# Performance work log

Measured on AMD Instinct MI355X. Metric: run time of the kernel, lower is better.

## Reference

```python
import jax, jax.numpy as jnp
import numpy as np

N, D = 8192, 1024

def setup_inputs() -> dict:
    key = jax.random.key(0)
    ks = jax.random.split(key, 7)
    s = 1.0 / np.sqrt(D)
    return {
        "sent_mat": jax.random.normal(ks[0], (N, D), dtype=jnp.float32),
        "indicator": 0,
        "Wq": jax.random.normal(ks[1], (D, D), dtype=jnp.float32) * s,
        "bq": jax.random.normal(ks[2], (D,), dtype=jnp.float32) * s,
        "Wk": jax.random.normal(ks[3], (D, D), dtype=jnp.float32) * s,
        "bk": jax.random.normal(ks[4], (D,), dtype=jnp.float32) * s,
        "Wv": jax.random.normal(ks[5], (D, D), dtype=jnp.float32) * s,
        "bv": jax.random.normal(ks[6], (D,), dtype=jnp.float32) * s,
    }

def reference(sent_mat, indicator, Wq, bq, Wk, bk, Wv, bv):
    # torch.nn.Linear: y = x @ W.T + b
    Q = sent_mat @ Wq.T + bq            # [N, D]
    K = sent_mat @ Wk.T + bk            # [N, D]
    V = sent_mat @ Wv.T + bv            # [N, D]
    sim = Q @ K.T                       # [N, N]
    if indicator == 0:                  # custom score inversion
        sim = 1.0 - sim
    sim_norm = sim / jnp.sqrt(jnp.asarray(D, dtype=sim.dtype))
    # NOTE: softmax over dim=0 (columns normalized over rows), unconventional
    attn_w = jax.nn.softmax(sim_norm, axis=0)   # [N, N]
    attn_out = attn_w @ V               # [N, D]
    return (attn_out, attn_w)
```

## Files before the change

### kernel.cpp

```cpp
#include <hip/hip_runtime.h>

#define NT 8192
#define DM 1024

typedef unsigned short u16;
typedef __bf16 bf16x8 __attribute__((ext_vector_type(8)));
typedef float f32x4 __attribute__((ext_vector_type(4)));
typedef u16 u16x8 __attribute__((ext_vector_type(8)));

__device__ __forceinline__ u16 f2bf(float f) {
  union { float f; unsigned u; } v; v.f = f;
  unsigned r = v.u + 0x7fffu + ((v.u >> 16) & 1u);
  return (u16)(r >> 16);
}
__device__ __forceinline__ float bf2f(u16 h) {
  union { unsigned u; float f; } v; v.u = ((unsigned)h) << 16;
  return v.f;
}

__device__ __forceinline__ void stage16(const u16* g, u16* lds_wave_uniform) {
  __builtin_amdgcn_global_load_lds(
      (const __attribute__((address_space(1))) unsigned int*)g,
      (__attribute__((address_space(3))) unsigned int*)lds_wave_uniform, 16, 0, 0);
}

__global__ void cvt_all_kernel(const float* __restrict__ X, const float* __restrict__ Wq,
                               const float* __restrict__ Wk, const float* __restrict__ Wv,
                               u16* __restrict__ Xb, u16* __restrict__ Wqb,
                               u16* __restrict__ Wkb, u16* __restrict__ Wvb) {
  const int NX = NT * DM / 4;
  const int NW = DM * DM / 4;
  const int total = NX + 3 * NW;
  int i = blockIdx.x * blockDim.x + threadIdx.x;
  int stride = gridDim.x * blockDim.x;
  for (; i < total; i += stride) {
    const float* src; u16* dst; int j;
    if (i < NX)               { src = X;  dst = Xb;  j = i; }
    else if (i < NX + NW)     { src = Wq; dst = Wqb; j = i - NX; }
    else if (i < NX + 2 * NW) { src = Wk; dst = Wkb; j = i - NX - NW; }
    else                      { src = Wv; dst = Wvb; j = i - NX - 2 * NW; }
    float4 v = reinterpret_cast<const float4*>(src)[j];
    ushort4 o;
    o.x = f2bf(v.x); o.y = f2bf(v.y); o.z = f2bf(v.z); o.w = f2bf(v.w);
    reinterpret_cast<ushort4*>(dst)[j] = o;
  }
}

__global__ __launch_bounds__(512, 2)
void qkt_exp_256(const u16* __restrict__ Q, const u16* __restrict__ Kmat, int K,
                 u16* __restrict__ E, float* __restrict__ cs,
                 const int* __restrict__ indp) {
  __shared__ u16 AT[2][256 * 64];
  __shared__ u16 BT[2][256 * 64];
  const int t = threadIdx.x;
  const int l = t & 63;
  const int w = t >> 6;
  const int wm = w >> 2;
  const int wn = w & 3;
  const int r16 = l & 15;
  const int half = l >> 4;

  const int gx = gridDim.x;
  const int nwg = gx * gridDim.y;
  int lin = blockIdx.y * gx + blockIdx.x;
  if ((nwg & 7) == 0) lin = (lin & 7) * (nwg >> 3) + (lin >> 3);
  const int bx = lin % gx;
  const int by = lin / gx;
  const size_t brow = (size_t)by * 256;
  const size_t bcol = (size_t)bx * 256;

  const int srow = w * 8 + (l >> 3);
  const int kel = ((l & 7) ^ (l >> 3)) * 8;
  const int ntiles = K >> 6;

  f32x4 acc[8][4] = {};

#pragma unroll
  for (int q = 0; q < 4; ++q) {
    stage16(Q    + (brow + q * 64 + srow) * (size_t)K + kel, &AT[0][q * 4096 + w * 512]);
    stage16(Kmat + (bcol + q * 64 + srow) * (size_t)K + kel, &BT[0][q * 4096 + w * 512]);
  }
  __syncthreads();

  for (int tt = 0; tt < ntiles; ++tt) {
    const int cur = tt & 1;
    const int nxt = cur ^ 1;
    const int k1 = (tt + 1) << 6;
    const bool more = (tt + 1 < ntiles);
#pragma unroll
    for (int p = 0; p < 4; ++p) {
      if (p == 0 && more) {
#pragma unroll
        for (int q = 0; q < 4; ++q)
          stage16(Q + (brow + q * 64 + srow) * (size_t)K + (k1 + kel),
                  &AT[nxt][q * 4096 + w * 512]);
      }
      if (p == 1 && more) {
#pragma unroll
        for (int q = 0; q < 4; ++q)
          stage16(Kmat + (bcol + q * 64 + srow) * (size_t)K + (k1 + kel),
                  &BT[nxt][q * 4096 + w * 512]);
      }
      bf16x8 af[4][2], bfr[2][2];
#pragma unroll
      for (int m = 0; m < 4; ++m) {
        const int row = wm * 128 + (p >> 1) * 64 + m * 16 + r16;
#pragma unroll
        for (int kk = 0; kk < 2; ++kk) {
          const int slot = (half + 4 * kk) ^ (r16 & 7);
          af[m][kk] = *reinterpret_cast<const bf16x8*>(&AT[cur][row * 64 + slot * 8]);
        }
      }
#pragma unroll
      for (int n = 0; n < 2; ++n) {
        const int row = wn * 64 + (p & 1) * 32 + n * 16 + r16;
#pragma unroll
        for (int kk = 0; kk < 2; ++kk) {
          const int slot = (half + 4 * kk) ^ (r16 & 7);
          bfr[n][kk] = *reinterpret_cast<const bf16x8*>(&BT[cur][row * 64 + slot * 8]);
        }
      }
      __builtin_amdgcn_s_setprio(1);
#pragma unroll
      for (int m = 0; m < 4; ++m)
#pragma unroll
        for (int n = 0; n < 2; ++n)
#pragma unroll
          for (int kk = 0; kk < 2; ++kk)
            acc[(p >> 1) * 4 + m][(p & 1) * 2 + n] = __builtin_amdgcn_mfma_f32_16x16x32_bf16(
                af[m][kk], bfr[n][kk], acc[(p >> 1) * 4 + m][(p & 1) * 2 + n], 0, 0, 0);
      __builtin_amdgcn_s_setprio(0);
      __builtin_amdgcn_sched_barrier(0);
    }
    __syncthreads();
  }

  const bool flip = (*indp == 0);
  const float cexp = 0.045084220027780106f;
  float csum[4] = {0.f, 0.f, 0.f, 0.f};
#pragma unroll
  for (int mg = 0; mg < 8; ++mg) {
#pragma unroll
    for (int ng = 0; ng < 4; ++ng) {
#pragma unroll
      for (int q = 0; q < 4; ++q) {
        float s = acc[mg][ng][q];
        float x = flip ? (1.0f - s) : s;
        float e = exp2f(x * cexp);
        size_t row = brow + wm * 128 + mg * 16 + half * 4 + q;
        size_t col = bcol + wn * 64 + ng * 16 + r16;
        E[row * NT + col] = f2bf(e);
        csum[ng] += e;
      }
    }
  }
#pragma unroll
  for (int ng = 0; ng < 4; ++ng) {
    float s = csum[ng];
    s += __shfl_xor(s, 16);
    s += __shfl_xor(s, 32);
    if (l < 16) atomicAdd(&cs[bcol + wn * 64 + ng * 16 + l], s);
  }
}

template<int EPI>
__global__ __launch_bounds__(512, 2)
void mega_bt(const u16* __restrict__ A, const u16* __restrict__ B, int K, int ldo,
             const float* __restrict__ bias, u16* __restrict__ obf,
             float* __restrict__ of32, float* __restrict__ cs,
             float* __restrict__ wf32, const int* __restrict__ indp) {
  __shared__ u16 AT[3][256 * 64];
  __shared__ u16 BT[3][128 * 64];
  const int t = threadIdx.x;
  const int l = t & 63;
  const int w = t >> 6;
  const int wm = w >> 2;
  const int wn = w & 3;
  const int r16 = l & 15;
  const int half = l >> 4;

  const int gx = gridDim.x;
  const int nwg = gx * gridDim.y;
  int lin = blockIdx.y * gx + blockIdx.x;
  if ((nwg & 7) == 0) lin = (lin & 7) * (nwg >> 3) + (lin >> 3);
  const int bx = lin % gx;
  const int by = lin / gx;
  const size_t brow = (size_t)by * 256;
  const size_t bcol = (size_t)bx * 128;

  const int srow = w * 8 + (l >> 3);
  const int kel = ((l & 7) ^ (l >> 3)) * 8;
  const int nt = K >> 6;

  f32x4 acc[8][2] = {};

#define STAGE(tile, buf)                                                              \
  {                                                                                   \
    const int k0_ = (tile) << 6;                                                      \
    _Pragma("unroll")                                                                 \
    for (int q = 0; q < 4; ++q)                                                       \
      stage16(A + (brow + q * 64 + srow) * (size_t)K + (k0_ + kel),                   \
              &AT[buf][q * 4096 + w * 512]);                                          \
    _Pragma("unroll")                                                                 \
    for (int q = 0; q < 2; ++q)                                                       \
      stage16(B + (bcol + q * 64 + srow) * (size_t)K + (k0_ + kel),                   \
              &BT[buf][q * 4096 + w * 512]);                                          \
  }

  STAGE(0, 0);
  STAGE(1, 1);

  for (int tt = 0; tt < nt; ++tt) {
    const int cur = tt % 3;
    if (tt < nt - 1) asm volatile("s_waitcnt vmcnt(6)" ::: "memory");
    else             asm volatile("s_waitcnt vmcnt(0)" ::: "memory");
    __builtin_amdgcn_s_barrier();
    __builtin_amdgcn_sched_barrier(0);
    if (tt + 2 < nt) STAGE(tt + 2, (tt + 2) % 3);
    __builtin_amdgcn_sched_barrier(0);

    bf16x8 bfr[2][2];
#pragma unroll
    for (int n = 0; n < 2; ++n) {
      const int row = wn * 32 + n * 16 + r16;
#pragma unroll
      for (int kk = 0; kk < 2; ++kk) {
        const int slot = (half + 4 * kk) ^ (r16 & 7);
        bfr[n][kk] = *reinterpret_cast<const bf16x8*>(&BT[cur][row * 64 + slot * 8]);
      }
    }
#pragma unroll
    for (int p = 0; p < 2; ++p) {
      bf16x8 af[4][2];
#pragma unroll
      for (int m = 0; m < 4; ++m) {
        const int row = wm * 128 + p * 64 + m * 16 + r16;
#pragma unroll
        for (int kk = 0; kk < 2; ++kk) {
          const int slot = (half + 4 * kk) ^ (r16 & 7);
          af[m][kk] = *reinterpret_cast<const bf16x8*>(&AT[cur][row * 64 + slot * 8]);
        }
      }
      __builtin_amdgcn_s_setprio(1);
#pragma unroll
      for (int m = 0; m < 4; ++m)
#pragma unroll
        for (int n = 0; n < 2; ++n)
#pragma unroll
          for (int kk = 0; kk < 2; ++kk)
            acc[p * 4 + m][n] = __builtin_amdgcn_mfma_f32_16x16x32_bf16(
                af[m][kk], bfr[n][kk], acc[p * 4 + m][n], 0, 0, 0);
      __builtin_amdgcn_s_setprio(0);
      __builtin_amdgcn_sched_barrier(0);
    }

    if constexpr (EPI == 3) {
      if ((tt >> 4) == bx) {
        const int kg = (tt << 6) + l;
        const float invc = 1.0f / cs[kg];
#pragma unroll
        for (int wi = 0; wi < 32; ++wi) {
          const int row = w * 32 + wi;
          const int slot = (l >> 3) ^ (row & 7);
          u16 ev = AT[cur][row * 64 + slot * 8 + (l & 7)];
          wf32[(brow + row) * (size_t)NT + kg] = bf2f(ev) * invc;
        }
      }
    }
  }
#undef STAGE

  if constexpr (EPI == 0) {
#pragma unroll
    for (int mg = 0; mg < 8; ++mg) {
#pragma unroll
      for (int n = 0; n < 2; ++n) {
        const int cc = wn * 32 + n * 16 + r16;
        const float bv = bias[bcol + cc];
#pragma unroll
        for (int q = 0; q < 4; ++q) {
          size_t row = brow + wm * 128 + mg * 16 + half * 4 + q;
          obf[row * (size_t)ldo + bcol + cc] = f2bf(acc[mg][n][q] + bv);
        }
      }
    }
  } else {
#pragma unroll
    for (int mg = 0; mg < 8; ++mg) {
#pragma unroll
      for (int n = 0; n < 2; ++n) {
#pragma unroll
        for (int q = 0; q < 4; ++q) {
          size_t row = brow + wm * 128 + mg * 16 + half * 4 + q;
          size_t col = bcol + wn * 32 + n * 16 + r16;
          of32[row * (size_t)ldo + col] = acc[mg][n][q];
        }
      }
    }
  }
}

template<int EPI, int AF32, int BF32>
__global__ __launch_bounds__(256)
void gemm_bt(const void* __restrict__ Av, const void* __restrict__ Bv, int K, int ldo,
             const float* __restrict__ bias, u16* __restrict__ obf,
             float* __restrict__ of32, const int* __restrict__ indp) {
  __shared__ u16 As[128 * 32];
  __shared__ u16 Bs[128 * 32];
  const int t = threadIdx.x;
  const int l = t & 63;
  const int w = t >> 6;
  const int wr = w >> 1;
  const int wc = w & 1;
  const int r16 = l & 15;
  const int half = l >> 4;

  const int gx = gridDim.x;
  const int nwg = gx * gridDim.y;
  int lin = blockIdx.y * gx + blockIdx.x;
  if ((nwg & 7) == 0) lin = (lin & 7) * (nwg >> 3) + (lin >> 3);
  const int bx = lin % gx;
  const int by = lin / gx;

  const size_t brow = (size_t)by * 128;
  const size_t bcol = (size_t)bx * 128;
  const int kel = (l & 3) * 8;
  const int lrow = l >> 2;

  f32x4 acc[4][4] = {};

  for (int k0 = 0; k0 < K; k0 += 32) {
#pragma unroll
    for (int c = 0; c < 2; ++c) {
      const int seg = c * 4 + w;
      const int r = seg * 16 + lrow;
      if constexpr (AF32) {
        const float* ga = (const float*)Av + (brow + r) * (size_t)K + (k0 + kel);
        float4 u0 = *reinterpret_cast<const float4*>(ga);
        float4 u1 = *reinterpret_cast<const float4*>(ga + 4);
        u16x8 o;
        o[0] = f2bf(u0.x); o[1] = f2bf(u0.y); o[2] = f2bf(u0.z); o[3] = f2bf(u0.w);
        o[4] = f2bf(u1.x); o[5] = f2bf(u1.y); o[6] = f2bf(u1.z); o[7] = f2bf(u1.w);
        *reinterpret_cast<u16x8*>(&As[seg * 512 + l * 8]) = o;
      } else {
        const u16* ga = (const u16*)Av + (brow + r) * (size_t)K + (k0 + kel);
        stage16(ga, &As[seg * 512]);
      }
      if constexpr (BF32) {
        const float* gb = (const float*)Bv + (bcol + r) * (size_t)K + (k0 + kel);
        float4 u0 = *reinterpret_cast<const float4*>(gb);
        float4 u1 = *reinterpret_cast<const float4*>(gb + 4);
        u16x8 o;
        o[0] = f2bf(u0.x); o[1] = f2bf(u0.y); o[2] = f2bf(u0.z); o[3] = f2bf(u0.w);
        o[4] = f2bf(u1.x); o[5] = f2bf(u1.y); o[6] = f2bf(u1.z); o[7] = f2bf(u1.w);
        *reinterpret_cast<u16x8*>(&Bs[seg * 512 + l * 8]) = o;
      } else {
        const u16* gb = (const u16*)Bv + (bcol + r) * (size_t)K + (k0 + kel);
        stage16(gb, &Bs[seg * 512]);
      }
    }
    __syncthreads();
    bf16x8 af[4], bfv[4];
#pragma unroll
    for (int m = 0; m < 4; ++m)
      af[m] = *reinterpret_cast<const bf16x8*>(&As[(wr * 64 + m * 16 + r16) * 32 + half * 8]);
#pragma unroll
    for (int n = 0; n < 4; ++n)
      bfv[n] = *reinterpret_cast<const bf16x8*>(&Bs[(wc * 64 + n * 16 + r16) * 32 + half * 8]);
#pragma unroll
    for (int m = 0; m < 4; ++m)
#pragma unroll
      for (int n = 0; n < 4; ++n)
        acc[m][n] = __builtin_amdgcn_mfma_f32_16x16x32_bf16(af[m], bfv[n], acc[m][n], 0, 0, 0);
    __syncthreads();
  }

  const int crow0 = wr * 64 + half * 4;
  const int ccol0 = wc * 64 + r16;

  if constexpr (EPI == 0) {
#pragma unroll
    for (int m = 0; m < 4; ++m) {
#pragma unroll
      for (int n = 0; n < 4; ++n) {
        const int cc = ccol0 + n * 16;
        const float bv = bias[bcol + cc];
#pragma unroll
        for (int q = 0; q < 4; ++q) {
          size_t idx = (brow + crow0 + m * 16 + q) * (size_t)ldo + (bcol + cc);
          obf[idx] = f2bf(acc[m][n][q] + bv);
        }
      }
    }
  } else if constexpr (EPI == 1) {
    const bool flip = (*indp == 0);
    const float cexp = 0.045084220027780106f;
#pragma unroll
    for (int m = 0; m < 4; ++m) {
#pragma unroll
      for (int n = 0; n < 4; ++n) {
        const int cc = ccol0 + n * 16;
#pragma unroll
        for (int q = 0; q < 4; ++q) {
          float s = acc[m][n][q];
          float x = flip ? (1.0f - s) : s;
          size_t idx = (brow + crow0 + m * 16 + q) * (size_t)ldo + (bcol + cc);
          of32[idx] = exp2f(x * cexp);
        }
      }
    }
  } else {
#pragma unroll
    for (int m = 0; m < 4; ++m) {
#pragma unroll
      for (int n = 0; n < 4; ++n) {
        const int cc = ccol0 + n * 16;
#pragma unroll
        for (int q = 0; q < 4; ++q) {
          size_t idx = (brow + crow0 + m * 16 + q) * (size_t)ldo + (bcol + cc);
          of32[idx] = acc[m][n][q];
        }
      }
    }
  }
}

__global__ void colsum_kernel(const float* __restrict__ E, float* __restrict__ cs) {
  const int col = blockIdx.x * 256 + threadIdx.x;
  const int r0 = blockIdx.y * 256;
  float s = 0.f;
  for (int r = r0; r < r0 + 256; ++r)
    s += E[(size_t)r * NT + col];
  atomicAdd(&cs[col], s);
}

__global__ void norm_kernel(float* __restrict__ w, const float* __restrict__ cs, int n4) {
  int i = blockIdx.x * blockDim.x + threadIdx.x;
  int stride = gridDim.x * blockDim.x;
  for (; i < n4; i += stride) {
    float4 v = reinterpret_cast<float4*>(w)[i];
    int j4 = i & (NT / 4 - 1);
    float4 c = reinterpret_cast<const float4*>(cs)[j4];
    v.x /= c.x; v.y /= c.y; v.z /= c.z; v.w /= c.w;
    reinterpret_cast<float4*>(w)[i] = v;
  }
}

__global__ void vt_kernel(const u16* __restrict__ Vb, const float* __restrict__ cs,
                          u16* __restrict__ Vt) {
  __shared__ u16 tile[64][65];
  const int jb = blockIdx.x * 64;
  const int db = blockIdx.y * 64;
  const int t = threadIdx.x;
  {
    const int d = t & 63;
    const int j0 = t >> 6;
    for (int jj = j0; jj < 64; jj += 4)
      tile[jj][d] = Vb[(size_t)(jb + jj) * DM + db + d];
  }
  __syncthreads();
  {
    const int j = t & 63;
    const int d0 = t >> 6;
    const float inv = cs ? (1.0f / cs[jb + j]) : 1.0f;
    for (int dd = d0; dd < 64; dd += 4) {
      u16 raw = tile[j][dd];
      Vt[(size_t)(db + dd) * NT + jb + j] = cs ? f2bf(bf2f(raw) * inv) : raw;
    }
  }
}

extern "C" void kernel_launch(void* const* d_in, const int* in_sizes, int n_in,
                              void* d_out, int out_size, void* d_ws, size_t ws_size,
                              hipStream_t stream) {
  const float* X  = (const float*)d_in[0];
  const int* indp = (const int*)d_in[1];
  const float* Wq = (const float*)d_in[2];
  const float* bq = (const float*)d_in[3];
  const float* Wk = (const float*)d_in[4];
  const float* bk = (const float*)d_in[5];
  const float* Wv = (const float*)d_in[6];
  const float* bv = (const float*)d_in[7];

  float* attn_out = (float*)d_out;
  float* attn_w   = (float*)d_out + (size_t)NT * DM;

  const size_t EB_BYTES = (size_t)NT * NT * 2;
  const size_t QKV_BYTES = (size_t)NT * DM * 2;
  const size_t need_fast = EB_BYTES + 4 * QKV_BYTES + NT * 4;

  if (ws_size >= need_fast) {
    char* ws = (char*)d_ws;
    u16* Eb = (u16*)ws;
    u16* Qb = (u16*)(ws + EB_BYTES);
    u16* Kb = Qb + (size_t)NT * DM;
    u16* Vb = Kb + (size_t)NT * DM;
    u16* Vt = Vb + (size_t)NT * DM;
    float* cs = (float*)(Vt + (size_t)NT * DM);
    u16* Xb  = Eb;
    u16* Wqb = Eb + (size_t)NT * DM;
    u16* Wkb = Wqb + (size_t)DM * DM;
    u16* Wvb = Wkb + (size_t)DM * DM;

    cvt_all_kernel<<<2048, 256, 0, stream>>>(X, Wq, Wk, Wv, Xb, Wqb, Wkb, Wvb);

    dim3 gqkv(DM / 128, NT / 256);
    mega_bt<0><<<gqkv, 512, 0, stream>>>(Xb, Wqb, DM, DM, bq, Qb, nullptr, nullptr, nullptr, nullptr);
    mega_bt<0><<<gqkv, 512, 0, stream>>>(Xb, Wkb, DM, DM, bk, Kb, nullptr, nullptr, nullptr, nullptr);
    mega_bt<0><<<gqkv, 512, 0, stream>>>(Xb, Wvb, DM, DM, bv, Vb, nullptr, nullptr, nullptr, nullptr);

    hipMemsetAsync(cs, 0, NT * sizeof(float), stream);
    qkt_exp_256<<<dim3(NT / 256, NT / 256), 512, 0, stream>>>(Qb, Kb, DM, Eb, cs, indp);

    vt_kernel<<<dim3(NT / 64, DM / 64), 256, 0, stream>>>(Vb, cs, Vt);

    mega_bt<3><<<dim3(DM / 128, NT / 256), 512, 0, stream>>>(
        Eb, Vt, NT, DM, nullptr, nullptr, attn_out, cs, attn_w, nullptr);
  } else {
    char* ws = (char*)d_ws;
    u16* Qb = (u16*)ws;  ws += QKV_BYTES;
    u16* Kb = (u16*)ws;  ws += QKV_BYTES;
    u16* Vb = (u16*)ws;  ws += QKV_BYTES;
    u16* Vt = (u16*)ws;  ws += QKV_BYTES;
    float* cs = (float*)ws;

    dim3 gqkv(DM / 128, NT / 128);
    gemm_bt<0, 1, 1><<<gqkv, 256, 0, stream>>>(X, Wq, DM, DM, bq, Qb, nullptr, nullptr);
    gemm_bt<0, 1, 1><<<gqkv, 256, 0, stream>>>(X, Wk, DM, DM, bk, Kb, nullptr, nullptr);
    gemm_bt<0, 1, 1><<<gqkv, 256, 0, stream>>>(X, Wv, DM, DM, bv, Vb, nullptr, nullptr);

    gemm_bt<1, 0, 0><<<dim3(NT / 128, NT / 128), 256, 0, stream>>>(
        Qb, Kb, DM, NT, nullptr, nullptr, attn_w, indp);

    hipMemsetAsync(cs, 0, NT * sizeof(float), stream);
    colsum_kernel<<<dim3(32, 32), 256, 0, stream>>>(attn_w, cs);
    norm_kernel<<<4096, 256, 0, stream>>>(attn_w, cs, NT * NT / 4);
    vt_kernel<<<dim3(NT / 64, DM / 64), 256, 0, stream>>>(Vb, nullptr, Vt);

    gemm_bt<2, 1, 0><<<dim3(DM / 128, NT / 128), 256, 0, stream>>>(
        attn_w, Vt, NT, DM, nullptr, nullptr, attn_out, nullptr);
  }
}
```

Measured before the change: 514.8 us.

## Unfuse attn_w normalization from PV GEMM, retile waves, hoist QK^T prefetch

Removes the EPI==3 path where the PV GEMM wrote the normalized fp32 attention weights from its LDS tile during the K loop, and moves that work into a separate elementwise kernel that reads the bf16 exponentials and divides by the column sums. The mega_bt wave layout changes from 2x4 waves with 128x32 per-wave tiles to 4x2 waves with 64x64 tiles, which raises B-fragment reuse per A load. In the QK^T exp kernel, all next-tile global-to-LDS loads are now issued together before the compute phases, and the per-phase scheduling barriers are dropped. The cost is an extra pass over the N x N bf16 buffer and the fp32 output in the new kernel, in exchange for a simpler GEMM inner loop.

Measured after the change: 508.2 us. No clear change (-1.3%).

```diff
diff --git a/kernel.cpp b/kernel.cpp
--- a/kernel.cpp
+++ b/kernel.cpp
@@ -86,21 +86,19 @@
     const int cur = tt & 1;
     const int nxt = cur ^ 1;
     const int k1 = (tt + 1) << 6;
-    const bool more = (tt + 1 < ntiles);
+    if (tt + 1 < ntiles) {
+#pragma unroll
+      for (int q = 0; q < 4; ++q)
+        stage16(Q + (brow + q * 64 + srow) * (size_t)K + (k1 + kel),
+                &AT[nxt][q * 4096 + w * 512]);
+#pragma unroll
+      for (int q = 0; q < 4; ++q)
+        stage16(Kmat + (bcol + q * 64 + srow) * (size_t)K + (k1 + kel),
+                &BT[nxt][q * 4096 + w * 512]);
+      __builtin_amdgcn_sched_barrier(0);
+    }
 #pragma unroll
     for (int p = 0; p < 4; ++p) {
-      if (p == 0 && more) {
-#pragma unroll
-        for (int q = 0; q < 4; ++q)
-          stage16(Q + (brow + q * 64 + srow) * (size_t)K + (k1 + kel),
-                  &AT[nxt][q * 4096 + w * 512]);
-      }
-      if (p == 1 && more) {
-#pragma unroll
-        for (int q = 0; q < 4; ++q)
-          stage16(Kmat + (bcol + q * 64 + srow) * (size_t)K + (k1 + kel),
-                  &BT[nxt][q * 4096 + w * 512]);
-      }
       bf16x8 af[4][2], bfr[2][2];
 #pragma unroll
       for (int m = 0; m < 4; ++m) {
@@ -130,7 +128,6 @@
             acc[(p >> 1) * 4 + m][(p & 1) * 2 + n] = __builtin_amdgcn_mfma_f32_16x16x32_bf16(
                 af[m][kk], bfr[n][kk], acc[(p >> 1) * 4 + m][(p & 1) * 2 + n], 0, 0, 0);
       __builtin_amdgcn_s_setprio(0);
-      __builtin_amdgcn_sched_barrier(0);
     }
     __syncthreads();
   }
@@ -167,15 +164,14 @@
 __global__ __launch_bounds__(512, 2)
 void mega_bt(const u16* __restrict__ A, const u16* __restrict__ B, int K, int ldo,
              const float* __restrict__ bias, u16* __restrict__ obf,
-             float* __restrict__ of32, float* __restrict__ cs,
-             float* __restrict__ wf32, const int* __restrict__ indp) {
+             float* __restrict__ of32) {
   __shared__ u16 AT[3][256 * 64];
   __shared__ u16 BT[3][128 * 64];
   const int t = threadIdx.x;
   const int l = t & 63;
   const int w = t >> 6;
-  const int wm = w >> 2;
-  const int wn = w & 3;
+  const int wm = w >> 1;
+  const int wn = w & 1;
   const int r16 = l & 15;
   const int half = l >> 4;
 
@@ -192,7 +188,7 @@
   const int kel = ((l & 7) ^ (l >> 3)) * 8;
   const int nt = K >> 6;
 
-  f32x4 acc[8][2] = {};
+  f32x4 acc[4][4] = {};
 
 #define STAGE(tile, buf)                                                              \
   {                                                                                   \
@@ -219,10 +215,10 @@
     if (tt + 2 < nt) STAGE(tt + 2, (tt + 2) % 3);
     __builtin_amdgcn_sched_barrier(0);
 
-    bf16x8 bfr[2][2];
-#pragma unroll
-    for (int n = 0; n < 2; ++n) {
-      const int row = wn * 32 + n * 16 + r16;
+    bf16x8 bfr[4][2];
+#pragma unroll
+    for (int n = 0; n < 4; ++n) {
+      const int row = wn * 64 + n * 16 + r16;
 #pragma unroll
       for (int kk = 0; kk < 2; ++kk) {
         const int slot = (half + 4 * kk) ^ (r16 & 7);
@@ -231,68 +227,53 @@
     }
 #pragma unroll
     for (int p = 0; p < 2; ++p) {
-      bf16x8 af[4][2];
-#pragma unroll
-      for (int m = 0; m < 4; ++m) {
-        const int row = wm * 128 + p * 64 + m * 16 + r16;
+      bf16x8 af[2][2];
+#pragma unroll
+      for (int m2 = 0; m2 < 2; ++m2) {
+        const int row = wm * 64 + (2 * p + m2) * 16 + r16;
 #pragma unroll
         for (int kk = 0; kk < 2; ++kk) {
           const int slot = (half + 4 * kk) ^ (r16 & 7);
-          af[m][kk] = *reinterpret_cast<const bf16x8*>(&AT[cur][row * 64 + slot * 8]);
+          af[m2][kk] = *reinterpret_cast<const bf16x8*>(&AT[cur][row * 64 + slot * 8]);
         }
       }
       __builtin_amdgcn_s_setprio(1);
 #pragma unroll
-      for (int m = 0; m < 4; ++m)
-#pragma unroll
-        for (int n = 0; n < 2; ++n)
+      for (int m2 = 0; m2 < 2; ++m2)
+#pragma unroll
+        for (int n = 0; n < 4; ++n)
 #pragma unroll
           for (int kk = 0; kk < 2; ++kk)
-            acc[p * 4 + m][n] = __builtin_amdgcn_mfma_f32_16x16x32_bf16(
-                af[m][kk], bfr[n][kk], acc[p * 4 + m][n], 0, 0, 0);
+            acc[2 * p + m2][n] = __builtin_amdgcn_mfma_f32_16x16x32_bf16(
+                af[m2][kk], bfr[n][kk], acc[2 * p + m2][n], 0, 0, 0);
       __builtin_amdgcn_s_setprio(0);
-      __builtin_amdgcn_sched_barrier(0);
-    }
-
-    if constexpr (EPI == 3) {
-      if ((tt >> 4) == bx) {
-        const int kg = (tt << 6) + l;
-        const float invc = 1.0f / cs[kg];
-#pragma unroll
-        for (int wi = 0; wi < 32; ++wi) {
-          const int row = w * 32 + wi;
-          const int slot = (l >> 3) ^ (row & 7);
-          u16 ev = AT[cur][row * 64 + slot * 8 + (l & 7)];
-          wf32[(brow + row) * (size_t)NT + kg] = bf2f(ev) * invc;
-        }
-      }
     }
   }
 #undef STAGE
 
   if constexpr (EPI == 0) {
 #pragma unroll
-    for (int mg = 0; mg < 8; ++mg) {
-#pragma unroll
-      for (int n = 0; n < 2; ++n) {
-        const int cc = wn * 32 + n * 16 + r16;
+    for (int mg = 0; mg < 4; ++mg) {
+#pragma unroll
+      for (int n = 0; n < 4; ++n) {
+        const int cc = wn * 64 + n * 16 + r16;
         const float bv = bias[bcol + cc];
 #pragma unroll
         for (int q = 0; q < 4; ++q) {
-          size_t row = brow + wm * 128 + mg * 16 + half * 4 + q;
+          size_t row = brow + wm * 64 + mg * 16 + half * 4 + q;
           obf[row * (size_t)ldo + bcol + cc] = f2bf(acc[mg][n][q] + bv);
         }
       }
     }
   } else {
 #pragma unroll
-    for (int mg = 0; mg < 8; ++mg) {
-#pragma unroll
-      for (int n = 0; n < 2; ++n) {
+    for (int mg = 0; mg < 4; ++mg) {
+#pragma unroll
+      for (int n = 0; n < 4; ++n) {
 #pragma unroll
         for (int q = 0; q < 4; ++q) {
-          size_t row = brow + wm * 128 + mg * 16 + half * 4 + q;
-          size_t col = bcol + wn * 32 + n * 16 + r16;
+          size_t row = brow + wm * 64 + mg * 16 + half * 4 + q;
+          size_t col = bcol + wn * 64 + n * 16 + r16;
           of32[row * (size_t)ldo + col] = acc[mg][n][q];
         }
       }
@@ -446,6 +427,23 @@
   }
 }
 
+__global__ void norm_bf16_kernel(const u16* __restrict__ e, float* __restrict__ w,
+                                 const float* __restrict__ cs, int n4) {
+  int i = blockIdx.x * blockDim.x + threadIdx.x;
+  int stride = gridDim.x * blockDim.x;
+  for (; i < n4; i += stride) {
+    ushort4 ev = reinterpret_cast<const ushort4*>(e)[i];
+    int j4 = i & (NT / 4 - 1);
+    float4 c = reinterpret_cast<const float4*>(cs)[j4];
+    float4 v;
+    v.x = bf2f(ev.x) / c.x;
+    v.y = bf2f(ev.y) / c.y;
+    v.z = bf2f(ev.z) / c.z;
+    v.w = bf2f(ev.w) / c.w;
+    reinterpret_cast<float4*>(w)[i] = v;
+  }
+}
+
 __global__ void vt_kernel(const u16* __restrict__ Vb, const float* __restrict__ cs,
                           u16* __restrict__ Vt) {
   __shared__ u16 tile[64][65];
@@ -505,17 +503,19 @@
     cvt_all_kernel<<<2048, 256, 0, stream>>>(X, Wq, Wk, Wv, Xb, Wqb, Wkb, Wvb);
 
     dim3 gqkv(DM / 128, NT / 256);
-    mega_bt<0><<<gqkv, 512, 0, stream>>>(Xb, Wqb, DM, DM, bq, Qb, nullptr, nullptr, nullptr, nullptr);
-    mega_bt<0><<<gqkv, 512, 0, stream>>>(Xb, Wkb, DM, DM, bk, Kb, nullptr, nullptr, nullptr, nullptr);
-    mega_bt<0><<<gqkv, 512, 0, stream>>>(Xb, Wvb, DM, DM, bv, Vb, nullptr, nullptr, nullptr, nullptr);
+    mega_bt<0><<<gqkv, 512, 0, stream>>>(Xb, Wqb, DM, DM, bq, Qb, nullptr);
+    mega_bt<0><<<gqkv, 512, 0, stream>>>(Xb, Wkb, DM, DM, bk, Kb, nullptr);
+    mega_bt<0><<<gqkv, 512, 0, stream>>>(Xb, Wvb, DM, DM, bv, Vb, nullptr);
 
     hipMemsetAsync(cs, 0, NT * sizeof(float), stream);
     qkt_exp_256<<<dim3(NT / 256, NT / 256), 512, 0, stream>>>(Qb, Kb, DM, Eb, cs, indp);
 
     vt_kernel<<<dim3(NT / 64, DM / 64), 256, 0, stream>>>(Vb, cs, Vt);
 
-    mega_bt<3><<<dim3(DM / 128, NT / 256), 512, 0, stream>>>(
-        Eb, Vt, NT, DM, nullptr, nullptr, attn_out, cs, attn_w, nullptr);
+    mega_bt<2><<<dim3(DM / 128, NT / 256), 512, 0, stream>>>(
+        Eb, Vt, NT, DM, nullptr, nullptr, attn_out);
+
+    norm_bf16_kernel<<<4096, 256, 0, stream>>>(Eb, attn_w, cs, NT * NT / 4);
   } else {
     char* ws = (char*)d_ws;
     u16* Qb = (u16*)ws;  ws += QKV_BYTES;
```
